# Kernel tuning notes

Measured on AMD Instinct MI355X. Metric: run time of the kernel, lower is better.

The kernel has to match this reference:

```python
import jax, jax.numpy as jnp
import numpy as np

EPS = 1e-5
GRID = (16, 16)
BLOCK = (16, 16)


def _ln(x):
    # LayerNorm over (C, H, W) per sample, affine = identity (fresh nn.LayerNorm each call)
    m = jnp.mean(x, axis=(1, 2, 3), keepdims=True)
    v = jnp.mean(jnp.square(x - m), axis=(1, 2, 3), keepdims=True)
    return (x - m) / jnp.sqrt(v + EPS)


def _gelu(x):
    return jax.nn.gelu(x, approximate=False)  # torch F.gelu default = exact erf


def _block(x, fh, fw):
    # NCHW -> [N, C, gh*gw, fh*fw]
    n, c, h, w = x.shape
    gh, gw = h // fh, w // fw
    return x.reshape(n, c, gh, fh, gw, fw).transpose(0, 1, 2, 4, 3, 5).reshape(n, c, gh * gw, fh * fw)


def _unblock(x, gh, gw, fh, fw):
    n, c, _, _ = x.shape
    return x.reshape(n, c, gh, gw, fh, fw).transpose(0, 1, 2, 4, 3, 5).reshape(n, c, gh * fh, gw * fw)


def _gating(x, w1, b1, w2, b2, w3, b3, w4, b4):
    # GetSpatialGatingWeights
    n, c, h, w = x.shape
    x = _ln(x)
    x = jnp.einsum('nchw,cd->ndhw', x, w1) + b1[None, :, None, None]  # C -> 2C
    x = _gelu(x)
    u, v = jnp.split(x, 2, axis=1)
    # grid MLP on u: mix across gh*gw grid positions
    gh, gw = GRID
    fh, fw = h // gh, w // gw
    u = _block(u, fh, fw)                                             # [n,c,G,P]
    u = jnp.einsum('ncgp,gd->ncdp', u, w2) + b2[None, None, :, None]
    u = _unblock(u, gh, gw, fh, fw)
    # block MLP on v: mix across fh*fw positions inside each block
    fh, fw = BLOCK
    gh, gw = h // fh, w // fw
    v = _block(v, fh, fw)
    v = jnp.einsum('ncgp,pd->ncgd', v, w3) + b3
    v = _unblock(v, gh, gw, fh, fw)
    x = jnp.concatenate([u, v], axis=1)
    return jnp.einsum('nchw,cd->ndhw', x, w4) + b4[None, :, None, None]  # 2C -> C


def _chan_lin(x, w, b):
    return jnp.einsum('nchw,cd->ndhw', x, w) + b[None, :, None, None]


def setup_inputs() -> dict:
    key = jax.random.key(0)
    ks = list(jax.random.split(key, 40))
    k = iter(ks)

    def rn(shape, s=0.02):
        return jax.random.normal(next(k), shape, dtype=jnp.float32) * s

    N, Cx, Cy, F, H, W = 8, 128, 256, 128, 128, 128
    G = GRID[0] * GRID[1]    # 256
    B = BLOCK[0] * BLOCK[1]  # 256
    inp = {
        'x': jax.random.normal(next(k), (N, Cx, H, W), dtype=jnp.float32),
        'y': jax.random.normal(next(k), (N, Cy, H // 2, W // 2), dtype=jnp.float32),
        'wt': rn((Cy, F, 2, 2)), 'bt': rn((F,)),
        'wc1': rn((Cx, F)), 'bc1': rn((F,)),
        'wc2': rn((F, F)), 'bc2': rn((F,)),
        'wl1': rn((F, F)), 'bl1': rn((F,)),
        'wl2': rn((F, F)), 'bl2': rn((F,)),
        'wl3': rn((F, F)), 'bl3': rn((F,)),
        'wl4': rn((F, F)), 'bl4': rn((F,)),
    }
    for p in ('g1', 'g2'):
        inp[p + '_w1'] = rn((F, 2 * F)); inp[p + '_b1'] = rn((2 * F,))
        inp[p + '_w2'] = rn((G, G));     inp[p + '_b2'] = rn((G,))
        inp[p + '_w3'] = rn((B, B));     inp[p + '_b3'] = rn((B,))
        inp[p + '_w4'] = rn((2 * F, F)); inp[p + '_b4'] = rn((F,))
    return inp


def reference(x, y, wt, bt, wc1, bc1, wc2, bc2, wl1, bl1, wl2, bl2, wl3, bl3, wl4, bl4,
              g1_w1, g1_b1, g1_w2, g1_b2, g1_w3, g1_b3, g1_w4, g1_b4,
              g2_w1, g2_b1, g2_w2, g2_b2, g2_w3, g2_b3, g2_w4, g2_b4):
    # ConvT_up: kernel=2, stride=2 (non-overlapping) + ReLU
    n, cy, hy, wy = y.shape
    fo = wt.shape[1]
    y = jnp.einsum('nchw,cokl->nohkwl', y, wt).reshape(n, fo, 2 * hy, 2 * wy) + bt[None, :, None, None]
    y = jax.nn.relu(y)
    # Conv1x1 (+ReLU) projections
    x = jax.nn.relu(_chan_lin(x, wc1, bc1))
    y = jax.nn.relu(_chan_lin(y, wc2, bc2))
    shortcut_x, shortcut_y = x, y
    # x branch
    x = _gelu(_chan_lin(_ln(x), wl1, bl1))
    gx = _gating(x, g1_w1, g1_b1, g1_w2, g1_b2, g1_w3, g1_b3, g1_w4, g1_b4)
    # y branch
    y = _gelu(_chan_lin(_ln(y), wl2, bl2))
    gy = _gating(y, g2_w1, g2_b1, g2_w2, g2_b2, g2_w3, g2_b3, g2_w4, g2_b4)
    # cross gating + residuals (dropout p=0.0 -> identity)
    y = _chan_lin(y * gx, wl3, bl3) + shortcut_y
    x = _chan_lin(x * gy, wl4, bl4) + y + shortcut_x
    return x, y
```

## Files before the change

### kernel.cpp

```cpp
#include <hip/hip_runtime.h>
#include <hip/hip_bf16.h>


typedef unsigned short u16;
typedef __bf16 bf16x8 __attribute__((ext_vector_type(8)));
typedef u16    u16x8  __attribute__((ext_vector_type(8)));
typedef u16    u16x4  __attribute__((ext_vector_type(4)));
typedef float  f32x4  __attribute__((ext_vector_type(4)));

__device__ __forceinline__ float bf2f(u16 u) {
  union { float f; unsigned int i; } v; v.i = ((unsigned int)u) << 16; return v.f;
}
__device__ __forceinline__ u16 f2bf(float f) {
  union { float f; unsigned int i; } v; v.f = f;
  unsigned int x = v.i;
  return (u16)((x + 0x7fffu + ((x >> 16) & 1u)) >> 16);
}
__device__ __forceinline__ f32x4 mfma16(u16x8 a, u16x8 b, f32x4 c) {
  return __builtin_amdgcn_mfma_f32_16x16x32_bf16(
      __builtin_bit_cast(bf16x8, a), __builtin_bit_cast(bf16x8, b), c, 0, 0, 0);
}
__device__ __forceinline__ float gelu_erf(float v) {
  return 0.5f * v * (1.0f + erff(v * 0.70710678118654752f));
}

__global__ __launch_bounds__(256) void prep_k(
    const float* __restrict__ wc1f, const float* __restrict__ wc2f,
    const float* __restrict__ wl1f, const float* __restrict__ wl2f,
    const float* __restrict__ wl3f, const float* __restrict__ wl4f,
    const float* __restrict__ g1w1, const float* __restrict__ g2w1,
    const float* __restrict__ g1w4, const float* __restrict__ g2w4,
    const float* __restrict__ g1w2, const float* __restrict__ g2w2,
    const float* __restrict__ g1w3, const float* __restrict__ g2w3,
    const float* __restrict__ wtf,
    u16* __restrict__ wb, float* __restrict__ cs, float* __restrict__ ps) {
  const int b = blockIdx.x, t = threadIdx.x;
  if (b < 384) {
    const float* src = b < 64 ? wc1f : b < 128 ? wc2f : b < 192 ? wl1f
                     : b < 256 ? wl2f : b < 320 ? wl3f : wl4f;
    const int w = b >> 6;
    const int i = ((b & 63) << 8) + t;
    const int d = i >> 7, c = i & 127;
    wb[w * 16384 + i] = f2bf(src[c * 128 + d]);
  } else if (b < 640) {
    const float* src = b < 512 ? g1w1 : g2w1;
    const int base = b < 512 ? 98304 : 131072;
    const int i = (((b - (b < 512 ? 384 : 512)) << 8) + t);
    const int d = i >> 7, c = i & 127;
    wb[base + i] = f2bf(src[c * 256 + d]);
  } else if (b < 896) {
    const float* src = b < 768 ? g1w4 : g2w4;
    const int base = b < 768 ? 163840 : 196608;
    const int i = (((b - (b < 768 ? 640 : 768)) << 8) + t);
    const int d = i >> 8, c = i & 255;
    wb[base + i] = f2bf(src[c * 128 + d]);
  } else if (b < 1920) {
    const int w = (b - 896) >> 8;
    const float* src = w == 0 ? g1w2 : w == 1 ? g2w2 : w == 2 ? g1w3 : g2w3;
    const int base = 229376 + w * 65536;
    const int i = (((b - 896) & 255) << 8) + t;
    const int d = i >> 8, g = i & 255;
    wb[base + i] = f2bf(src[g * 256 + d]);
  } else if (b < 2432) {
    const int i = ((b - 1920) << 8) + t;
    const int c = i & 255, r = i >> 8, o = r & 127, kl = r >> 7;
    wb[491520 + i] = f2bf(wtf[(c * 128 + o) * 4 + kl]);
  } else if (b < 2436) {
    const int w = b - 2432;
    const float* src = w == 0 ? wl1f : w == 1 ? wl2f : w == 2 ? g1w1 : g2w1;
    const int cout = w < 2 ? 128 : 256;
    if (t < cout) {
      float s = 0.f;
      for (int c = 0; c < 128; ++c) s += bf2f(f2bf(src[c * cout + t]));
      cs[w * 256 + t] = s;
    }
  } else {
    if (t < 64) ps[t] = 0.f;
  }
}

__global__ __launch_bounds__(256, 2) void gemmX_k(
    const float* __restrict__ X, const u16* __restrict__ Wt,
    const float* __restrict__ bias, u16* __restrict__ out,
    float* __restrict__ pso) {
  __shared__ u16 As[128 * 136];
  __shared__ float red[8];
  const int tid = threadIdx.x;
  const int m0 = blockIdx.x * 128;
  const int ns = m0 >> 14, pb = m0 & 16383;
  const int wid = tid >> 6, lane = tid & 63, fr = lane & 15, fg = lane >> 4;
  const int wmt = (wid & 1) * 64, wnc = (wid >> 1) * 64;

#pragma unroll
  for (int it = 0; it < 16; ++it) {
    const int idx = it * 256 + tid;
    const int c = idx & 127, t4 = idx >> 7;
    const f32x4 v = *(const f32x4*)(X + (((size_t)(ns * 128 + c)) << 14) + pb + t4 * 4);
#pragma unroll
    for (int r = 0; r < 4; ++r) As[(t4 * 4 + r) * 136 + c] = f2bf(v[r]);
  }
  __syncthreads();

  f32x4 acc[4][4] = {};
  const u16* Brow = Wt + (size_t)(wnc + fr) * 128;
  u16x8 a[4][4];
#pragma unroll
  for (int ks = 0; ks < 4; ++ks) {
    const int kb = ks * 32 + fg * 8;
#pragma unroll
    for (int i = 0; i < 4; ++i)
      a[ks][i] = *(const u16x8*)(As + (wmt + i * 16 + fr) * 136 + kb);
  }
#pragma unroll
  for (int ks = 0; ks < 4; ++ks) {
    const int kb = ks * 32 + fg * 8;
    u16x8 b_[4];
#pragma unroll
    for (int j = 0; j < 4; ++j)
      b_[j] = *(const u16x8*)(Brow + (size_t)j * 16 * 128 + kb);
#pragma unroll
    for (int i = 0; i < 4; ++i)
#pragma unroll
      for (int j = 0; j < 4; ++j) acc[i][j] = mfma16(b_[j], a[ks][i], acc[i][j]);
  }

  float s1 = 0.f, s2 = 0.f;
#pragma unroll
  for (int i = 0; i < 4; ++i) {
    const int token = m0 + wmt + i * 16 + fr;
#pragma unroll
    for (int j = 0; j < 4; ++j) {
      const int ch0 = wnc + j * 16 + fg * 4;
      const f32x4 bz = *(const f32x4*)(bias + ch0);
      f32x4 v = acc[i][j];
      u16x4 sv;
#pragma unroll
      for (int r = 0; r < 4; ++r) {
        v[r] = fmaxf(v[r] + bz[r], 0.f);
        s1 += v[r]; s2 += v[r] * v[r];
        sv[r] = f2bf(v[r]);
      }
      *(u16x4*)(out + (size_t)token * 128 + ch0) = sv;
    }
  }
#pragma unroll
  for (int off = 32; off > 0; off >>= 1) {
    s1 += __shfl_down(s1, off); s2 += __shfl_down(s2, off);
  }
  if (lane == 0) { red[wid] = s1; red[4 + wid] = s2; }
  __syncthreads();
  if (tid == 0)  atomicAdd(&pso[2 * ns],     red[0] + red[1] + red[2] + red[3]);
  if (tid == 64) atomicAdd(&pso[2 * ns + 1], red[4] + red[5] + red[6] + red[7]);
}

__global__ __launch_bounds__(256, 2) void gemmY2_k(
    const float* __restrict__ Y, const u16* __restrict__ Wtb,
    const float* __restrict__ bt, const u16* __restrict__ Wc2,
    const float* __restrict__ bc2, u16* __restrict__ out,
    float* __restrict__ pso) {
  __shared__ u16 As[64 * 256];
  __shared__ u16 Cs[64 * 136];
  __shared__ float red[8];
  const int tid = threadIdx.x;
  const int m0 = blockIdx.x * 64;
  const int ns = m0 >> 12, pb = m0 & 4095;
  const int wid = tid >> 6, lane = tid & 63, fr = lane & 15, fg = lane >> 4;
  const int tokg = (wid & 1) * 32;
  const int chg  = (wid >> 1) * 64;
  const int xorl = (fr & 7) << 4;

#pragma unroll
  for (int it = 0; it < 16; ++it) {
    const int idx = it * 256 + tid;
    const int c = idx & 255, t4 = idx >> 8;
    const f32x4 v = *(const f32x4*)(Y + (((size_t)(ns * 256 + c)) << 12) + pb + t4 * 4);
#pragma unroll
    for (int r = 0; r < 4; ++r) {
      const int tok = t4 * 4 + r;
      const int byte = (tok * 512 + c * 2) ^ ((tok & 7) << 4);
      *(u16*)((char*)As + byte) = f2bf(v[r]);
    }
  }
  __syncthreads();

  float s1 = 0.f, s2 = 0.f;
  for (int kl = 0; kl < 4; ++kl) {
    if (kl) __syncthreads();
    f32x4 acc1[2][4] = {};
    {
      const u16* Brow = Wtb + (size_t)(kl * 128 + chg + fr) * 256;
#pragma unroll
      for (int ks = 0; ks < 8; ++ks) {
        const int kb = ks * 32 + fg * 8;
        u16x8 a_[2], b_[4];
#pragma unroll
        for (int i = 0; i < 2; ++i) {
          const int tok = tokg + i * 16 + fr;
          const int byte = (tok * 512 + kb * 2) ^ xorl;
          a_[i] = *(const u16x8*)((const char*)As + byte);
        }
#pragma unroll
        for (int j = 0; j < 4; ++j)
          b_[j] = *(const u16x8*)(Brow + (size_t)j * 16 * 256 + kb);
#pragma unroll
        for (int i = 0; i < 2; ++i)
#pragma unroll
          for (int j = 0; j < 4; ++j) acc1[i][j] = mfma16(b_[j], a_[i], acc1[i][j]);
      }
    }
#pragma unroll
    for (int i = 0; i < 2; ++i) {
      const int tok = tokg + i * 16 + fr;
#pragma unroll
      for (int j = 0; j < 4; ++j) {
        const int o0 = chg + j * 16 + fg * 4;
        const f32x4 bz = *(const f32x4*)(bt + o0);
        u16x4 sv;
#pragma unroll
        for (int r = 0; r < 4; ++r) sv[r] = f2bf(fmaxf(acc1[i][j][r] + bz[r], 0.f));
        *(u16x4*)(Cs + tok * 136 + o0) = sv;
      }
    }
    __syncthreads();
    f32x4 acc2[2][4] = {};
    {
      const u16* Brow = Wc2 + (size_t)(chg + fr) * 128;
#pragma unroll
      for (int ks = 0; ks < 4; ++ks) {
        const int kb = ks * 32 + fg * 8;
        u16x8 a_[2], b_[4];
#pragma unroll
        for (int i = 0; i < 2; ++i)
          a_[i] = *(const u16x8*)(Cs + (tokg + i * 16 + fr) * 136 + kb);
#pragma unroll
        for (int j = 0; j < 4; ++j)
          b_[j] = *(const u16x8*)(Brow + (size_t)j * 16 * 128 + kb);
#pragma unroll
        for (int i = 0; i < 2; ++i)
#pragma unroll
          for (int j = 0; j < 4; ++j) acc2[i][j] = mfma16(b_[j], a_[i], acc2[i][j]);
      }
    }
#pragma unroll
    for (int i = 0; i < 2; ++i) {
      const int ytok = m0 + tokg + i * 16 + fr;
      const int hy = (ytok >> 6) & 63, wy = ytok & 63;
      const int opix = ((ns * 128 + 2 * hy + (kl >> 1)) << 7) + 2 * wy + (kl & 1);
#pragma unroll
      for (int j = 0; j < 4; ++j) {
        const int ch0 = chg + j * 16 + fg * 4;
        const f32x4 bz = *(const f32x4*)(bc2 + ch0);
        u16x4 sv;
#pragma unroll
        for (int r = 0; r < 4; ++r) {
          float v = fmaxf(acc2[i][j][r] + bz[r], 0.f);
          s1 += v; s2 += v * v;
          sv[r] = f2bf(v);
        }
        *(u16x4*)(out + (size_t)opix * 128 + ch0) = sv;
      }
    }
  }
#pragma unroll
  for (int off = 32; off > 0; off >>= 1) {
    s1 += __shfl_down(s1, off); s2 += __shfl_down(s2, off);
  }
  if (lane == 0) { red[wid] = s1; red[4 + wid] = s2; }
  __syncthreads();
  if (tid == 0)  atomicAdd(&pso[2 * ns],     red[0] + red[1] + red[2] + red[3]);
  if (tid == 64) atomicAdd(&pso[2 * ns + 1], red[4] + red[5] + red[6] + red[7]);
}

__global__ __launch_bounds__(256, 2) void gemm4d_k(
    const u16* __restrict__ Ay, const u16* __restrict__ Ax,
    const u16* __restrict__ Wty, const u16* __restrict__ Wtx,
    const float* __restrict__ by, const float* __restrict__ bx,
    float* __restrict__ ps,
    const float* __restrict__ csy, const float* __restrict__ csx,
    u16* __restrict__ oy, u16* __restrict__ ox) {
  __shared__ float red[8];
  const int br = blockIdx.y;
  const u16* A1 = br ? Ax : Ay;
  const u16* Wt = br ? Wtx : Wty;
  const float* bias = br ? bx : by;
  const float* pst = ps + (br ? 0 : 16);
  float* pso = ps + (br ? 32 : 48);
  const float* cs = br ? csx : csy;
  u16* out = br ? ox : oy;

  const int tid = threadIdx.x;
  const int m0 = blockIdx.x * 128;
  const int wid = tid >> 6, lane = tid & 63, fr = lane & 15, fg = lane >> 4;
  const int wmt = (wid & 1) * 64, wnc = (wid >> 1) * 64;

  f32x4 acc[4][4] = {};
  const u16* Arow = A1 + (size_t)(m0 + wmt + fr) * 128;
  const u16* Brow = Wt + (size_t)(wnc + fr) * 128;

  u16x8 a[4][4];
#pragma unroll
  for (int ks = 0; ks < 4; ++ks) {
    const int kb = ks * 32 + fg * 8;
#pragma unroll
    for (int i = 0; i < 4; ++i)
      a[ks][i] = *(const u16x8*)(Arow + (size_t)i * 16 * 128 + kb);
  }
#pragma unroll
  for (int ks = 0; ks < 4; ++ks) {
    const int kb = ks * 32 + fg * 8;
    u16x8 b_[4];
#pragma unroll
    for (int j = 0; j < 4; ++j)
      b_[j] = *(const u16x8*)(Brow + (size_t)j * 16 * 128 + kb);
#pragma unroll
    for (int i = 0; i < 4; ++i)
#pragma unroll
      for (int j = 0; j < 4; ++j) acc[i][j] = mfma16(b_[j], a[ks][i], acc[i][j]);
  }

  const int s = m0 >> 14;
  const float inv_n = 1.f / 2097152.f;
  const float mean = pst[2 * s] * inv_n;
  const float var = pst[2 * s + 1] * inv_n - mean * mean;
  const float alpha = rsqrtf(var + 1e-5f);
  const float beta = -mean * alpha;

  float s1 = 0.f, s2 = 0.f;
#pragma unroll
  for (int i = 0; i < 4; ++i) {
    const int token = m0 + wmt + i * 16 + fr;
#pragma unroll
    for (int j = 0; j < 4; ++j) {
      const int ch0 = wnc + j * 16 + fg * 4;
      const f32x4 bz = *(const f32x4*)(bias + ch0);
      const f32x4 csv = *(const f32x4*)(cs + ch0);
      f32x4 v = acc[i][j];
      u16x4 sv;
#pragma unroll
      for (int r = 0; r < 4; ++r) {
        v[r] = v[r] * alpha + beta * csv[r] + bz[r];
        v[r] = gelu_erf(v[r]);
        s1 += v[r]; s2 += v[r] * v[r];
        sv[r] = f2bf(v[r]);
      }
      *(u16x4*)(out + (size_t)token * 128 + ch0) = sv;
    }
  }
#pragma unroll
  for (int off = 32; off > 0; off >>= 1) {
    s1 += __shfl_down(s1, off); s2 += __shfl_down(s2, off);
  }
  if (lane == 0) { red[wid] = s1; red[4 + wid] = s2; }
  __syncthreads();
  if (tid == 0)  atomicAdd(&pso[2 * s],     red[0] + red[1] + red[2] + red[3]);
  if (tid == 64) atomicAdd(&pso[2 * s + 1], red[4] + red[5] + red[6] + red[7]);
}

template <int MODE>
__global__ __launch_bounds__(512, 2) void mlp3c_k(
    const u16* __restrict__ a1y, const u16* __restrict__ a1x,
    const u16* __restrict__ w1y, const u16* __restrict__ w1x,
    const float* __restrict__ b1y, const float* __restrict__ b1x,
    const float* __restrict__ ps,
    const float* __restrict__ csy, const float* __restrict__ csx,
    const u16* __restrict__ w2y, const u16* __restrict__ w2x,
    const float* __restrict__ b2y, const float* __restrict__ b2x,
    const u16* __restrict__ w4y, const u16* __restrict__ w4x,
    const float* __restrict__ b4y, const float* __restrict__ b4x,
    u16* __restrict__ goy, u16* __restrict__ gox) {
  __shared__ u16 Ts[34816];
  const int br = blockIdx.z;
  const u16* y1 = br ? a1x : a1y;
  const u16* w1b = br ? w1x : w1y;
  const float* b1 = br ? b1x : b1y;
  const float* pst = ps + (br ? 32 : 48);
  const float* csb = br ? csx : csy;
  const u16* w2b = br ? w2x : w2y;
  const float* b2 = br ? b2x : b2y;
  const u16* w4b = br ? w4x : w4y;
  const float* b4 = br ? b4x : b4y;
  u16* gout = br ? gox : goy;

  const int q2 = blockIdx.x, ns = blockIdx.y;
  const int tid = threadIdx.x;
  constexpr int coff = MODE ? 128 : 0;
  const int wid = tid >> 6, lane = tid & 63, fr = lane & 15, fg = lane >> 4;
  const int xorl = (fr & 7) << 4;

  int pbase, prow, pcol;
  if constexpr (MODE == 0) {
    pbase = ns * 16384 + (q2 >> 3) * 128 + (q2 & 7);
    prow = 1024; pcol = 8;
  } else {
    pbase = ns * 16384 + (q2 >> 3) * 2048 + (q2 & 7) * 16;
    prow = 128; pcol = 1;
  }
  auto pix = [&](int q) { return pbase + (q >> 4) * prow + (q & 15) * pcol; };

  {
    const int wgt = (wid >> 1) * 64;
    const int wc  = (wid & 1) * 64;
    const float inv_n = 1.f / 2097152.f;
    const float mean = pst[2 * ns] * inv_n;
    const float var = pst[2 * ns + 1] * inv_n - mean * mean;
    const float alpha = rsqrtf(var + 1e-5f);
    const float beta = -mean * alpha;

    f32x4 acc[4][4] = {};
    const u16* ar[4];
#pragma unroll
    for (int i = 0; i < 4; ++i)
      ar[i] = y1 + (size_t)pix(wgt + i * 16 + fr) * 128;
    const u16* br_ = w1b + (size_t)(coff + wc + fr) * 128;

    u16x8 a[4][4];
#pragma unroll
    for (int ks = 0; ks < 4; ++ks) {
      const int kb = ks * 32 + fg * 8;
#pragma unroll
      for (int i = 0; i < 4; ++i) a[ks][i] = *(const u16x8*)(ar[i] + kb);
    }
#pragma unroll
    for (int ks = 0; ks < 4; ++ks) {
      const int kb = ks * 32 + fg * 8;
      u16x8 b_[4];
#pragma unroll
      for (int j = 0; j < 4; ++j)
        b_[j] = *(const u16x8*)(br_ + (size_t)j * 16 * 128 + kb);
#pragma unroll
      for (int i = 0; i < 4; ++i)
#pragma unroll
        for (int j = 0; j < 4; ++j) acc[i][j] = mfma16(a[ks][i], b_[j], acc[i][j]);
    }
#pragma unroll
    for (int j = 0; j < 4; ++j) {
      const int c = wc + j * 16 + fr;
      const float cv = csb[coff + c];
      const float bz = b1[coff + c];
#pragma unroll
      for (int i = 0; i < 4; ++i) {
        const int g0 = wgt + i * 16 + fg * 4;
        u16x4 sv;
#pragma unroll
        for (int r = 0; r < 4; ++r)
          sv[r] = f2bf(gelu_erf(acc[i][j][r] * alpha + beta * cv + bz));
        const int byte = (c * 512 + g0 * 2) ^ xorl;
        *(u16x4*)((char*)Ts + byte) = sv;
      }
    }
  }
  __syncthreads();

  f32x4 accB[4][4];
  const int wcs = (wid >> 2) * 64;
  const int wds = (wid & 3) * 64;
  {
#pragma unroll
    for (int i = 0; i < 4; ++i)
#pragma unroll
      for (int j = 0; j < 4; ++j) accB[i][j] = f32x4{0.f, 0.f, 0.f, 0.f};
    const u16* br_ = w2b + (size_t)(wds + fr) * 256;
#pragma unroll
    for (int h = 0; h < 2; ++h) {
      u16x8 a[4][4];
#pragma unroll
      for (int ks = 0; ks < 4; ++ks) {
        const int kb = (h * 4 + ks) * 32 + fg * 8;
#pragma unroll
        for (int i = 0; i < 4; ++i) {
          const int c = wcs + i * 16 + fr;
          const int byte = (c * 512 + kb * 2) ^ xorl;
          a[ks][i] = *(const u16x8*)((const char*)Ts + byte);
        }
      }
#pragma unroll
      for (int ks = 0; ks < 4; ++ks) {
        const int kb = (h * 4 + ks) * 32 + fg * 8;
        u16x8 b_[4];
#pragma unroll
        for (int j = 0; j < 4; ++j)
          b_[j] = *(const u16x8*)(br_ + (size_t)j * 16 * 256 + kb);
#pragma unroll
        for (int i = 0; i < 4; ++i)
#pragma unroll
          for (int j = 0; j < 4; ++j) accB[i][j] = mfma16(a[ks][i], b_[j], accB[i][j]);
      }
    }
  }
  __syncthreads();

#pragma unroll
  for (int j = 0; j < 4; ++j) {
    const int d = wds + j * 16 + fr;
    const float bz = b2[d];
#pragma unroll
    for (int i = 0; i < 4; ++i) {
      const int c0 = wcs + i * 16 + fg * 4;
      u16x4 sv;
#pragma unroll
      for (int r = 0; r < 4; ++r) sv[r] = f2bf(accB[i][j][r] + bz);
      *(u16x4*)(Ts + d * 136 + c0) = sv;
    }
  }
  __syncthreads();

  {
    const int wp = (wid >> 1) * 64;
    const int wo = (wid & 1) * 64;
    f32x4 accC[4][4] = {};
    const u16* br_ = w4b + (size_t)(wo + fr) * 256 + coff;
#pragma unroll
    for (int ks = 0; ks < 4; ++ks) {
      const int kb = ks * 32 + fg * 8;
      u16x8 a_[4], b_[4];
#pragma unroll
      for (int i = 0; i < 4; ++i)
        a_[i] = *(const u16x8*)(Ts + (wp + i * 16 + fr) * 136 + kb);
#pragma unroll
      for (int j = 0; j < 4; ++j)
        b_[j] = *(const u16x8*)(br_ + (size_t)j * 16 * 256 + kb);
#pragma unroll
      for (int i = 0; i < 4; ++i)
#pragma unroll
        for (int j = 0; j < 4; ++j) accC[i][j] = mfma16(b_[j], a_[i], accC[i][j]);
    }
#pragma unroll
    for (int i = 0; i < 4; ++i) {
      const size_t pg = (size_t)pix(wp + i * 16 + fr) * 128;
#pragma unroll
      for (int j = 0; j < 4; ++j) {
        const int o0 = wo + j * 16 + fg * 4;
        f32x4 v = accC[i][j];
        u16x4 sv;
        if constexpr (MODE == 0) {
          const f32x4 bz = *(const f32x4*)(b4 + o0);
#pragma unroll
          for (int r = 0; r < 4; ++r) sv[r] = f2bf(v[r] + bz[r]);
        } else {
          const u16x4 pv = *(const u16x4*)(gout + pg + o0);
#pragma unroll
          for (int r = 0; r < 4; ++r) sv[r] = f2bf(v[r] + bf2f(pv[r]));
        }
        *(u16x4*)(gout + pg + o0) = sv;
      }
    }
  }
}

__global__ __launch_bounds__(256, 2) void dual5_k(
    const u16* __restrict__ y1, const u16* __restrict__ gx,
    const u16* __restrict__ x1, const u16* __restrict__ gy,
    const u16* __restrict__ w3b, const u16* __restrict__ w4b,
    const float* __restrict__ b3, const float* __restrict__ b4,
    const u16* __restrict__ y0, const u16* __restrict__ x0,
    float* __restrict__ outy, float* __restrict__ outx) {
  const int tid = threadIdx.x;
  const int m0 = blockIdx.x * 128;
  const int wid = tid >> 6, lane = tid & 63, fr = lane & 15, fg = lane >> 4;
  const int wmt = (wid & 1) * 64, wnc = (wid >> 1) * 64;

  f32x4 acc[4][4] = {};
  u16x4 y9[4][4];

  {
    const u16* Arow  = y1 + (size_t)(m0 + wmt + fr) * 128;
    const u16* Arow2 = gx + (size_t)(m0 + wmt + fr) * 128;
    const u16* Brow  = w3b + (size_t)(wnc + fr) * 128;
    u16x8 a[4][4], a2[4][4];
#pragma unroll
    for (int ks = 0; ks < 4; ++ks) {
      const int kb = ks * 32 + fg * 8;
#pragma unroll
      for (int i = 0; i < 4; ++i) {
        a[ks][i]  = *(const u16x8*)(Arow  + (size_t)i * 16 * 128 + kb);
        a2[ks][i] = *(const u16x8*)(Arow2 + (size_t)i * 16 * 128 + kb);
      }
    }
#pragma unroll
    for (int ks = 0; ks < 4; ++ks) {
      const int kb = ks * 32 + fg * 8;
      u16x8 b_[4];
#pragma unroll
      for (int j = 0; j < 4; ++j) b_[j] = *(const u16x8*)(Brow + (size_t)j * 16 * 128 + kb);
      u16x8 am[4];
#pragma unroll
      for (int i = 0; i < 4; ++i)
#pragma unroll
        for (int j = 0; j < 8; ++j) am[i][j] = f2bf(bf2f(a[ks][i][j]) * bf2f(a2[ks][i][j]));
#pragma unroll
      for (int i = 0; i < 4; ++i)
#pragma unroll
        for (int j = 0; j < 4; ++j) acc[i][j] = mfma16(b_[j], am[i], acc[i][j]);
    }
  }
  {
    u16x4 scv[4][4];
#pragma unroll
    for (int i = 0; i < 4; ++i) {
      const int token = m0 + wmt + i * 16 + fr;
#pragma unroll
      for (int j = 0; j < 4; ++j)
        scv[i][j] = *(const u16x4*)(y0 + (size_t)token * 128 + wnc + j * 16 + fg * 4);
    }
#pragma unroll
    for (int i = 0; i < 4; ++i) {
      const int token = m0 + wmt + i * 16 + fr;
      const int ns = token >> 14, p = token & 16383;
#pragma unroll
      for (int j = 0; j < 4; ++j) {
        const int ch0 = wnc + j * 16 + fg * 4;
        const f32x4 bz = *(const f32x4*)(b3 + ch0);
        f32x4 v = acc[i][j];
#pragma unroll
        for (int r = 0; r < 4; ++r) {
          v[r] += bz[r] + bf2f(scv[i][j][r]);
          outy[((size_t)(ns * 128 + ch0 + r) << 14) + p] = v[r];
          y9[i][j][r] = f2bf(v[r]);
        }
        acc[i][j] = f32x4{0.f, 0.f, 0.f, 0.f};
      }
    }
  }
  {
    const u16* Arow  = x1 + (size_t)(m0 + wmt + fr) * 128;
    const u16* Arow2 = gy + (size_t)(m0 + wmt + fr) * 128;
    const u16* Brow  = w4b + (size_t)(wnc + fr) * 128;
    u16x8 a[4][4], a2[4][4];
#pragma unroll
    for (int ks = 0; ks < 4; ++ks) {
      const int kb = ks * 32 + fg * 8;
#pragma unroll
      for (int i = 0; i < 4; ++i) {
        a[ks][i]  = *(const u16x8*)(Arow  + (size_t)i * 16 * 128 + kb);
        a2[ks][i] = *(const u16x8*)(Arow2 + (size_t)i * 16 * 128 + kb);
      }
    }
#pragma unroll
    for (int ks = 0; ks < 4; ++ks) {
      const int kb = ks * 32 + fg * 8;
      u16x8 b_[4];
#pragma unroll
      for (int j = 0; j < 4; ++j) b_[j] = *(const u16x8*)(Brow + (size_t)j * 16 * 128 + kb);
      u16x8 am[4];
#pragma unroll
      for (int i = 0; i < 4; ++i)
#pragma unroll
        for (int j = 0; j < 8; ++j) am[i][j] = f2bf(bf2f(a[ks][i][j]) * bf2f(a2[ks][i][j]));
#pragma unroll
      for (int i = 0; i < 4; ++i)
#pragma unroll
        for (int j = 0; j < 4; ++j) acc[i][j] = mfma16(b_[j], am[i], acc[i][j]);
    }
  }
  {
    u16x4 scv[4][4];
#pragma unroll
    for (int i = 0; i < 4; ++i) {
      const int token = m0 + wmt + i * 16 + fr;
#pragma unroll
      for (int j = 0; j < 4; ++j)
        scv[i][j] = *(const u16x4*)(x0 + (size_t)token * 128 + wnc + j * 16 + fg * 4);
    }
#pragma unroll
    for (int i = 0; i < 4; ++i) {
      const int token = m0 + wmt + i * 16 + fr;
      const int ns = token >> 14, p = token & 16383;
#pragma unroll
      for (int j = 0; j < 4; ++j) {
        const int ch0 = wnc + j * 16 + fg * 4;
        const f32x4 bz = *(const f32x4*)(b4 + ch0);
        f32x4 v = acc[i][j];
#pragma unroll
        for (int r = 0; r < 4; ++r) {
          v[r] += bz[r] + bf2f(y9[i][j][r]) + bf2f(scv[i][j][r]);
          outx[((size_t)(ns * 128 + ch0 + r) << 14) + p] = v[r];
        }
      }
    }
  }
}

extern "C" void kernel_launch(void* const* d_in, const int* in_sizes, int n_in,
                              void* d_out, int out_size, void* d_ws, size_t ws_size,
                              hipStream_t stream) {
  (void)in_sizes; (void)n_in; (void)out_size; (void)ws_size;
  const float* xf   = (const float*)d_in[0];
  const float* yf   = (const float*)d_in[1];
  const float* wtf  = (const float*)d_in[2];
  const float* btf  = (const float*)d_in[3];
  const float* wc1f = (const float*)d_in[4];
  const float* bc1f = (const float*)d_in[5];
  const float* wc2f = (const float*)d_in[6];
  const float* bc2f = (const float*)d_in[7];
  const float* wl1f = (const float*)d_in[8];
  const float* bl1f = (const float*)d_in[9];
  const float* wl2f = (const float*)d_in[10];
  const float* bl2f = (const float*)d_in[11];
  const float* wl3f = (const float*)d_in[12];
  const float* bl3f = (const float*)d_in[13];
  const float* wl4f = (const float*)d_in[14];
  const float* bl4f = (const float*)d_in[15];
  const float* g1w1 = (const float*)d_in[16];
  const float* g1b1 = (const float*)d_in[17];
  const float* g1w2 = (const float*)d_in[18];
  const float* g1b2 = (const float*)d_in[19];
  const float* g1w3 = (const float*)d_in[20];
  const float* g1b3 = (const float*)d_in[21];
  const float* g1w4 = (const float*)d_in[22];
  const float* g1b4 = (const float*)d_in[23];
  const float* g2w1 = (const float*)d_in[24];
  const float* g2b1 = (const float*)d_in[25];
  const float* g2w2 = (const float*)d_in[26];
  const float* g2b2 = (const float*)d_in[27];
  const float* g2w3 = (const float*)d_in[28];
  const float* g2b3 = (const float*)d_in[29];
  const float* g2w4 = (const float*)d_in[30];
  const float* g2b4 = (const float*)d_in[31];

  constexpr int T16 = 16777216;
  u16* WS  = (u16*)d_ws;
  u16* x0b = WS;
  u16* x1b = WS + (size_t)T16;
  u16* y0b = WS + (size_t)2 * T16;
  u16* y1b = WS + (size_t)3 * T16;
  u16* gyb = WS + (size_t)4 * T16;
  u16* gxb = WS + (size_t)5 * T16;
  float* fb = (float*)(WS + (size_t)6 * T16);
  float* cs = fb;
  float* ps = fb + 1024;
  u16* wb   = (u16*)(fb + 1024 + 64);
  float* ps0 = ps, *ps1 = ps + 16;

  const u16* wc1b = wb;
  const u16* wc2b = wb + 16384;
  const u16* wl1b = wb + 32768;
  const u16* wl2b = wb + 49152;
  const u16* wl3b = wb + 65536;
  const u16* wl4b = wb + 81920;
  const u16* g1w1b = wb + 98304;
  const u16* g2w1b = wb + 131072;
  const u16* g1w4b = wb + 163840;
  const u16* g2w4b = wb + 196608;
  const u16* g1w2b = wb + 229376;
  const u16* g2w2b = wb + 294912;
  const u16* g1w3b = wb + 360448;
  const u16* g2w3b = wb + 425984;
  const u16* wtb   = wb + 491520;

  float* outx = (float*)d_out;
  float* outy = (float*)d_out + (size_t)T16;

  const dim3 B256(256), B512(512);

  prep_k<<<dim3(2437), B256, 0, stream>>>(
      wc1f, wc2f, wl1f, wl2f, wl3f, wl4f, g1w1, g2w1, g1w4, g2w4,
      g1w2, g2w2, g1w3, g2w3, wtf, wb, cs, ps);

  gemmY2_k<<<dim3(512), B256, 0, stream>>>(yf, wtb, btf, wc2b, bc2f, y0b, ps1);
  gemmX_k<<<dim3(1024), B256, 0, stream>>>(xf, wc1b, bc1f, x0b, ps0);

  gemm4d_k<<<dim3(1024, 2), B256, 0, stream>>>(
      y0b, x0b, wl2b, wl1b, bl2f, bl1f, ps, cs + 256, cs, y1b, x1b);

  mlp3c_k<0><<<dim3(64, 8, 2), B512, 0, stream>>>(
      y1b, x1b, g2w1b, g1w1b, g2b1, g1b1, ps, cs + 768, cs + 512,
      g2w2b, g1w2b, g2b2, g1b2, g2w4b, g1w4b, g2b4, g1b4, gyb, gxb);
  mlp3c_k<1><<<dim3(64, 8, 2), B512, 0, stream>>>(
      y1b, x1b, g2w1b, g1w1b, g2b1, g1b1, ps, cs + 768, cs + 512,
      g2w3b, g1w3b, g2b3, g1b3, g2w4b, g1w4b, g2b4, g1b4, gyb, gxb);

  dual5_k<<<dim3(1024), B256, 0, stream>>>(
      y1b, gxb, x1b, gyb, wl3b, wl4b, bl3f, bl4f, y0b, x0b, outy, outx);
}
```

Before: 535.2 us.

## Merge input projection kernels and fold gating multiply into gating epilogue

The separate y (convT+conv1x1) and x (conv1x1) projection kernels become one launch with 1536 blocks, branching on block index, so the two independent workloads share the GPU. The cross-gating multiply (y1*gx, x1*gy) moves from the final dual GEMM's inner loop into the epilogue of the second gating-MLP pass, which writes the gated product directly. The final kernel then reads one activation tensor per branch instead of two and skips the per-element bf16 multiply. The cost is an extra read in the gating epilogue, plus one more bf16 rounding step before the multiply.

After: 517.5 us. 3.3% less time.

```diff
diff --git a/kernel.cpp b/kernel.cpp
--- a/kernel.cpp
+++ b/kernel.cpp
@@ -79,196 +79,195 @@
   }
 }
 
-__global__ __launch_bounds__(256, 2) void gemmX_k(
-    const float* __restrict__ X, const u16* __restrict__ Wt,
-    const float* __restrict__ bias, u16* __restrict__ out,
-    float* __restrict__ pso) {
-  __shared__ u16 As[128 * 136];
+__global__ __launch_bounds__(256, 2) void gemmYX_k(
+    const float* __restrict__ Y, const float* __restrict__ X,
+    const u16* __restrict__ Wtb, const float* __restrict__ bt,
+    const u16* __restrict__ Wc2, const float* __restrict__ bc2,
+    const u16* __restrict__ Wc1, const float* __restrict__ bc1,
+    u16* __restrict__ oy, u16* __restrict__ ox, float* __restrict__ ps) {
+  __shared__ u16 sm[25088];
   __shared__ float red[8];
   const int tid = threadIdx.x;
-  const int m0 = blockIdx.x * 128;
-  const int ns = m0 >> 14, pb = m0 & 16383;
   const int wid = tid >> 6, lane = tid & 63, fr = lane & 15, fg = lane >> 4;
-  const int wmt = (wid & 1) * 64, wnc = (wid >> 1) * 64;
-
-#pragma unroll
-  for (int it = 0; it < 16; ++it) {
-    const int idx = it * 256 + tid;
-    const int c = idx & 127, t4 = idx >> 7;
-    const f32x4 v = *(const f32x4*)(X + (((size_t)(ns * 128 + c)) << 14) + pb + t4 * 4);
-#pragma unroll
-    for (int r = 0; r < 4; ++r) As[(t4 * 4 + r) * 136 + c] = f2bf(v[r]);
-  }
-  __syncthreads();
-
-  f32x4 acc[4][4] = {};
-  const u16* Brow = Wt + (size_t)(wnc + fr) * 128;
-  u16x8 a[4][4];
-#pragma unroll
-  for (int ks = 0; ks < 4; ++ks) {
-    const int kb = ks * 32 + fg * 8;
-#pragma unroll
-    for (int i = 0; i < 4; ++i)
-      a[ks][i] = *(const u16x8*)(As + (wmt + i * 16 + fr) * 136 + kb);
-  }
-#pragma unroll
-  for (int ks = 0; ks < 4; ++ks) {
-    const int kb = ks * 32 + fg * 8;
-    u16x8 b_[4];
-#pragma unroll
-    for (int j = 0; j < 4; ++j)
-      b_[j] = *(const u16x8*)(Brow + (size_t)j * 16 * 128 + kb);
-#pragma unroll
-    for (int i = 0; i < 4; ++i)
-#pragma unroll
-      for (int j = 0; j < 4; ++j) acc[i][j] = mfma16(b_[j], a[ks][i], acc[i][j]);
-  }
-
-  float s1 = 0.f, s2 = 0.f;
-#pragma unroll
-  for (int i = 0; i < 4; ++i) {
-    const int token = m0 + wmt + i * 16 + fr;
-#pragma unroll
-    for (int j = 0; j < 4; ++j) {
-      const int ch0 = wnc + j * 16 + fg * 4;
-      const f32x4 bz = *(const f32x4*)(bias + ch0);
-      f32x4 v = acc[i][j];
-      u16x4 sv;
+
+  if (blockIdx.x < 512) {
+    u16* As = sm;
+    u16* Cs = sm + 16384;
+    float* pso = ps + 16;
+    const int m0 = blockIdx.x * 64;
+    const int ns = m0 >> 12, pb = m0 & 4095;
+    const int tokg = (wid & 1) * 32;
+    const int chg  = (wid >> 1) * 64;
+    const int xorl = (fr & 7) << 4;
+
+#pragma unroll
+    for (int it = 0; it < 16; ++it) {
+      const int idx = it * 256 + tid;
+      const int c = idx & 255, t4 = idx >> 8;
+      const f32x4 v = *(const f32x4*)(Y + (((size_t)(ns * 256 + c)) << 12) + pb + t4 * 4);
 #pragma unroll
       for (int r = 0; r < 4; ++r) {
-        v[r] = fmaxf(v[r] + bz[r], 0.f);
-        s1 += v[r]; s2 += v[r] * v[r];
-        sv[r] = f2bf(v[r]);
-      }
-      *(u16x4*)(out + (size_t)token * 128 + ch0) = sv;
-    }
-  }
-#pragma unroll
-  for (int off = 32; off > 0; off >>= 1) {
-    s1 += __shfl_down(s1, off); s2 += __shfl_down(s2, off);
-  }
-  if (lane == 0) { red[wid] = s1; red[4 + wid] = s2; }
-  __syncthreads();
-  if (tid == 0)  atomicAdd(&pso[2 * ns],     red[0] + red[1] + red[2] + red[3]);
-  if (tid == 64) atomicAdd(&pso[2 * ns + 1], red[4] + red[5] + red[6] + red[7]);
-}
-
-__global__ __launch_bounds__(256, 2) void gemmY2_k(
-    const float* __restrict__ Y, const u16* __restrict__ Wtb,
-    const float* __restrict__ bt, const u16* __restrict__ Wc2,
-    const float* __restrict__ bc2, u16* __restrict__ out,
-    float* __restrict__ pso) {
-  __shared__ u16 As[64 * 256];
-  __shared__ u16 Cs[64 * 136];
-  __shared__ float red[8];
-  const int tid = threadIdx.x;
-  const int m0 = blockIdx.x * 64;
-  const int ns = m0 >> 12, pb = m0 & 4095;
-  const int wid = tid >> 6, lane = tid & 63, fr = lane & 15, fg = lane >> 4;
-  const int tokg = (wid & 1) * 32;
-  const int chg  = (wid >> 1) * 64;
-  const int xorl = (fr & 7) << 4;
-
-#pragma unroll
-  for (int it = 0; it < 16; ++it) {
-    const int idx = it * 256 + tid;
-    const int c = idx & 255, t4 = idx >> 8;
-    const f32x4 v = *(const f32x4*)(Y + (((size_t)(ns * 256 + c)) << 12) + pb + t4 * 4);
-#pragma unroll
-    for (int r = 0; r < 4; ++r) {
-      const int tok = t4 * 4 + r;
-      const int byte = (tok * 512 + c * 2) ^ ((tok & 7) << 4);
-      *(u16*)((char*)As + byte) = f2bf(v[r]);
-    }
-  }
-  __syncthreads();
-
-  float s1 = 0.f, s2 = 0.f;
-  for (int kl = 0; kl < 4; ++kl) {
-    if (kl) __syncthreads();
-    f32x4 acc1[2][4] = {};
-    {
-      const u16* Brow = Wtb + (size_t)(kl * 128 + chg + fr) * 256;
-#pragma unroll
-      for (int ks = 0; ks < 8; ++ks) {
-        const int kb = ks * 32 + fg * 8;
-        u16x8 a_[2], b_[4];
-#pragma unroll
-        for (int i = 0; i < 2; ++i) {
-          const int tok = tokg + i * 16 + fr;
-          const int byte = (tok * 512 + kb * 2) ^ xorl;
-          a_[i] = *(const u16x8*)((const char*)As + byte);
-        }
-#pragma unroll
-        for (int j = 0; j < 4; ++j)
-          b_[j] = *(const u16x8*)(Brow + (size_t)j * 16 * 256 + kb);
-#pragma unroll
-        for (int i = 0; i < 2; ++i)
-#pragma unroll
-          for (int j = 0; j < 4; ++j) acc1[i][j] = mfma16(b_[j], a_[i], acc1[i][j]);
-      }
-    }
-#pragma unroll
-    for (int i = 0; i < 2; ++i) {
-      const int tok = tokg + i * 16 + fr;
+        const int tok = t4 * 4 + r;
+        const int byte = (tok * 512 + c * 2) ^ ((tok & 7) << 4);
+        *(u16*)((char*)As + byte) = f2bf(v[r]);
+      }
+    }
+    __syncthreads();
+
+    float s1 = 0.f, s2 = 0.f;
+    for (int kl = 0; kl < 4; ++kl) {
+      if (kl) __syncthreads();
+      f32x4 acc1[2][4] = {};
+      {
+        const u16* Brow = Wtb + (size_t)(kl * 128 + chg + fr) * 256;
+#pragma unroll
+        for (int ks = 0; ks < 8; ++ks) {
+          const int kb = ks * 32 + fg * 8;
+          u16x8 a_[2], b_[4];
+#pragma unroll
+          for (int i = 0; i < 2; ++i) {
+            const int tok = tokg + i * 16 + fr;
+            const int byte = (tok * 512 + kb * 2) ^ xorl;
+            a_[i] = *(const u16x8*)((const char*)As + byte);
+          }
+#pragma unroll
+          for (int j = 0; j < 4; ++j)
+            b_[j] = *(const u16x8*)(Brow + (size_t)j * 16 * 256 + kb);
+#pragma unroll
+          for (int i = 0; i < 2; ++i)
+#pragma unroll
+            for (int j = 0; j < 4; ++j) acc1[i][j] = mfma16(b_[j], a_[i], acc1[i][j]);
+        }
+      }
+#pragma unroll
+      for (int i = 0; i < 2; ++i) {
+        const int tok = tokg + i * 16 + fr;
+#pragma unroll
+        for (int j = 0; j < 4; ++j) {
+          const int o0 = chg + j * 16 + fg * 4;
+          const f32x4 bz = *(const f32x4*)(bt + o0);
+          u16x4 sv;
+#pragma unroll
+          for (int r = 0; r < 4; ++r) sv[r] = f2bf(fmaxf(acc1[i][j][r] + bz[r], 0.f));
+          *(u16x4*)(Cs + tok * 136 + o0) = sv;
+        }
+      }
+      __syncthreads();
+      f32x4 acc2[2][4] = {};
+      {
+        const u16* Brow = Wc2 + (size_t)(chg + fr) * 128;
+#pragma unroll
+        for (int ks = 0; ks < 4; ++ks) {
+          const int kb = ks * 32 + fg * 8;
+          u16x8 a_[2], b_[4];
+#pragma unroll
+          for (int i = 0; i < 2; ++i)
+            a_[i] = *(const u16x8*)(Cs + (tokg + i * 16 + fr) * 136 + kb);
+#pragma unroll
+          for (int j = 0; j < 4; ++j)
+            b_[j] = *(const u16x8*)(Brow + (size_t)j * 16 * 128 + kb);
+#pragma unroll
+          for (int i = 0; i < 2; ++i)
+#pragma unroll
+            for (int j = 0; j < 4; ++j) acc2[i][j] = mfma16(b_[j], a_[i], acc2[i][j]);
+        }
+      }
+#pragma unroll
+      for (int i = 0; i < 2; ++i) {
+        const int ytok = m0 + tokg + i * 16 + fr;
+        const int hy = (ytok >> 6) & 63, wy = ytok & 63;
+        const int opix = ((ns * 128 + 2 * hy + (kl >> 1)) << 7) + 2 * wy + (kl & 1);
+#pragma unroll
+        for (int j = 0; j < 4; ++j) {
+          const int ch0 = chg + j * 16 + fg * 4;
+          const f32x4 bz = *(const f32x4*)(bc2 + ch0);
+          u16x4 sv;
+#pragma unroll
+          for (int r = 0; r < 4; ++r) {
+            float v = fmaxf(acc2[i][j][r] + bz[r], 0.f);
+            s1 += v; s2 += v * v;
+            sv[r] = f2bf(v);
+          }
+          *(u16x4*)(oy + (size_t)opix * 128 + ch0) = sv;
+        }
+      }
+    }
+#pragma unroll
+    for (int off = 32; off > 0; off >>= 1) {
+      s1 += __shfl_down(s1, off); s2 += __shfl_down(s2, off);
+    }
+    if (lane == 0) { red[wid] = s1; red[4 + wid] = s2; }
+    __syncthreads();
+    if (tid == 0)  atomicAdd(&pso[2 * ns],     red[0] + red[1] + red[2] + red[3]);
+    if (tid == 64) atomicAdd(&pso[2 * ns + 1], red[4] + red[5] + red[6] + red[7]);
+  } else {
+    u16* As = sm;
+    float* pso = ps;
+    const int m0 = (blockIdx.x - 512) * 128;
+    const int ns = m0 >> 14, pb = m0 & 16383;
+    const int wmt = (wid & 1) * 64, wnc = (wid >> 1) * 64;
+
+#pragma unroll
+    for (int it = 0; it < 16; ++it) {
+      const int idx = it * 256 + tid;
+      const int c = idx & 127, t4 = idx >> 7;
+      const f32x4 v = *(const f32x4*)(X + (((size_t)(ns * 128 + c)) << 14) + pb + t4 * 4);
+#pragma unroll
+      for (int r = 0; r < 4; ++r) As[(t4 * 4 + r) * 136 + c] = f2bf(v[r]);
+    }
+    __syncthreads();
+
+    f32x4 acc[4][4] = {};
+    const u16* Brow = Wc1 + (size_t)(wnc + fr) * 128;
+    u16x8 a[4][4];
+#pragma unroll
+    for (int ks = 0; ks < 4; ++ks) {
+      const int kb = ks * 32 + fg * 8;
+#pragma unroll
+      for (int i = 0; i < 4; ++i)
+        a[ks][i] = *(const u16x8*)(As + (wmt + i * 16 + fr) * 136 + kb);
+    }
+#pragma unroll
+    for (int ks = 0; ks < 4; ++ks) {
+      const int kb = ks * 32 + fg * 8;
+      u16x8 b_[4];
+#pragma unroll
+      for (int j = 0; j < 4; ++j)
+        b_[j] = *(const u16x8*)(Brow + (size_t)j * 16 * 128 + kb);
+#pragma unroll
+      for (int i = 0; i < 4; ++i)
+#pragma unroll
+        for (int j = 0; j < 4; ++j) acc[i][j] = mfma16(b_[j], a[ks][i], acc[i][j]);
+    }
+
+    float s1 = 0.f, s2 = 0.f;
+#pragma unroll
+    for (int i = 0; i < 4; ++i) {
+      const int token = m0 + wmt + i * 16 + fr;
 #pragma unroll
       for (int j = 0; j < 4; ++j) {
-        const int o0 = chg + j * 16 + fg * 4;
-        const f32x4 bz = *(const f32x4*)(bt + o0);
+        const int ch0 = wnc + j * 16 + fg * 4;
+        const f32x4 bz = *(const f32x4*)(bc1 + ch0);
+        f32x4 v = acc[i][j];
         u16x4 sv;
 #pragma unroll
-        for (int r = 0; r < 4; ++r) sv[r] = f2bf(fmaxf(acc1[i][j][r] + bz[r], 0.f));
-        *(u16x4*)(Cs + tok * 136 + o0) = sv;
-      }
-    }
+        for (int r = 0; r < 4; ++r) {
+          v[r] = fmaxf(v[r] + bz[r], 0.f);
+          s1 += v[r]; s2 += v[r] * v[r];
+          sv[r] = f2bf(v[r]);
+        }
+        *(u16x4*)(ox + (size_t)token * 128 + ch0) = sv;
+      }
+    }
+#pragma unroll
+    for (int off = 32; off > 0; off >>= 1) {
+      s1 += __shfl_down(s1, off); s2 += __shfl_down(s2, off);
+    }
+    if (lane == 0) { red[wid] = s1; red[4 + wid] = s2; }
     __syncthreads();
-    f32x4 acc2[2][4] = {};
-    {
-      const u16* Brow = Wc2 + (size_t)(chg + fr) * 128;
-#pragma unroll
-      for (int ks = 0; ks < 4; ++ks) {
-        const int kb = ks * 32 + fg * 8;
-        u16x8 a_[2], b_[4];
-#pragma unroll
-        for (int i = 0; i < 2; ++i)
-          a_[i] = *(const u16x8*)(Cs + (tokg + i * 16 + fr) * 136 + kb);
-#pragma unroll
-        for (int j = 0; j < 4; ++j)
-          b_[j] = *(const u16x8*)(Brow + (size_t)j * 16 * 128 + kb);
-#pragma unroll
-        for (int i = 0; i < 2; ++i)
-#pragma unroll
-          for (int j = 0; j < 4; ++j) acc2[i][j] = mfma16(b_[j], a_[i], acc2[i][j]);
-      }
-    }
-#pragma unroll
-    for (int i = 0; i < 2; ++i) {
-      const int ytok = m0 + tokg + i * 16 + fr;
-      const int hy = (ytok >> 6) & 63, wy = ytok & 63;
-      const int opix = ((ns * 128 + 2 * hy + (kl >> 1)) << 7) + 2 * wy + (kl & 1);
-#pragma unroll
-      for (int j = 0; j < 4; ++j) {
-        const int ch0 = chg + j * 16 + fg * 4;
-        const f32x4 bz = *(const f32x4*)(bc2 + ch0);
-        u16x4 sv;
-#pragma unroll
-        for (int r = 0; r < 4; ++r) {
-          float v = fmaxf(acc2[i][j][r] + bz[r], 0.f);
-          s1 += v; s2 += v * v;
-          sv[r] = f2bf(v);
-        }
-        *(u16x4*)(out + (size_t)opix * 128 + ch0) = sv;
-      }
-    }
-  }
-#pragma unroll
-  for (int off = 32; off > 0; off >>= 1) {
-    s1 += __shfl_down(s1, off); s2 += __shfl_down(s2, off);
-  }
-  if (lane == 0) { red[wid] = s1; red[4 + wid] = s2; }
-  __syncthreads();
-  if (tid == 0)  atomicAdd(&pso[2 * ns],     red[0] + red[1] + red[2] + red[3]);
-  if (tid == 64) atomicAdd(&pso[2 * ns + 1], red[4] + red[5] + red[6] + red[7]);
+    if (tid == 0)  atomicAdd(&pso[2 * ns],     red[0] + red[1] + red[2] + red[3]);
+    if (tid == 64) atomicAdd(&pso[2 * ns + 1], red[4] + red[5] + red[6] + red[7]);
+  }
 }
 
 __global__ __launch_bounds__(256, 2) void gemm4d_k(
@@ -371,6 +370,7 @@
   __shared__ u16 Ts[34816];
   const int br = blockIdx.z;
   const u16* y1 = br ? a1x : a1y;
+  const u16* mulp = br ? a1y : a1x;
   const u16* w1b = br ? w1x : w1y;
   const float* b1 = br ? b1x : b1y;
   const float* pst = ps + (br ? 32 : 48);
@@ -538,8 +538,10 @@
           for (int r = 0; r < 4; ++r) sv[r] = f2bf(v[r] + bz[r]);
         } else {
           const u16x4 pv = *(const u16x4*)(gout + pg + o0);
-#pragma unroll
-          for (int r = 0; r < 4; ++r) sv[r] = f2bf(v[r] + bf2f(pv[r]));
+          const u16x4 mv = *(const u16x4*)(mulp + pg + o0);
+#pragma unroll
+          for (int r = 0; r < 4; ++r)
+            sv[r] = f2bf((v[r] + bf2f(pv[r])) * bf2f(mv[r]));
         }
         *(u16x4*)(gout + pg + o0) = sv;
       }
@@ -548,8 +550,7 @@
 }
 
 __global__ __launch_bounds__(256, 2) void dual5_k(
-    const u16* __restrict__ y1, const u16* __restrict__ gx,
-    const u16* __restrict__ x1, const u16* __restrict__ gy,
+    const u16* __restrict__ y1g, const u16* __restrict__ x1g,
     const u16* __restrict__ w3b, const u16* __restrict__ w4b,
     const float* __restrict__ b3, const float* __restrict__ b4,
     const u16* __restrict__ y0, const u16* __restrict__ x0,
@@ -563,18 +564,15 @@
   u16x4 y9[4][4];
 
   {
-    const u16* Arow  = y1 + (size_t)(m0 + wmt + fr) * 128;
-    const u16* Arow2 = gx + (size_t)(m0 + wmt + fr) * 128;
-    const u16* Brow  = w3b + (size_t)(wnc + fr) * 128;
-    u16x8 a[4][4], a2[4][4];
-#pragma unroll
-    for (int ks = 0; ks < 4; ++ks) {
-      const int kb = ks * 32 + fg * 8;
-#pragma unroll
-      for (int i = 0; i < 4; ++i) {
-        a[ks][i]  = *(const u16x8*)(Arow  + (size_t)i * 16 * 128 + kb);
-        a2[ks][i] = *(const u16x8*)(Arow2 + (size_t)i * 16 * 128 + kb);
-      }
+    const u16* Arow = y1g + (size_t)(m0 + wmt + fr) * 128;
+    const u16* Brow = w3b + (size_t)(wnc + fr) * 128;
+    u16x8 a[4][4];
+#pragma unroll
+    for (int ks = 0; ks < 4; ++ks) {
+      const int kb = ks * 32 + fg * 8;
+#pragma unroll
+      for (int i = 0; i < 4; ++i)
+        a[ks][i] = *(const u16x8*)(Arow + (size_t)i * 16 * 128 + kb);
     }
 #pragma unroll
     for (int ks = 0; ks < 4; ++ks) {
@@ -582,15 +580,10 @@
       u16x8 b_[4];
 #pragma unroll
       for (int j = 0; j < 4; ++j) b_[j] = *(const u16x8*)(Brow + (size_t)j * 16 * 128 + kb);
-      u16x8 am[4];
-#pragma unroll
-      for (int i = 0; i < 4; ++i)
-#pragma unroll
-        for (int j = 0; j < 8; ++j) am[i][j] = f2bf(bf2f(a[ks][i][j]) * bf2f(a2[ks][i][j]));
-#pragma unroll
-      for (int i = 0; i < 4; ++i)
-#pragma unroll
-        for (int j = 0; j < 4; ++j) acc[i][j] = mfma16(b_[j], am[i], acc[i][j]);
+#pragma unroll
+      for (int i = 0; i < 4; ++i)
+#pragma unroll
+        for (int j = 0; j < 4; ++j) acc[i][j] = mfma16(b_[j], a[ks][i], acc[i][j]);
     }
   }
   {
@@ -622,18 +615,15 @@
     }
   }
   {
-    const u16* Arow  = x1 + (size_t)(m0 + wmt + fr) * 128;
-    const u16* Arow2 = gy + (size_t)(m0 + wmt + fr) * 128;
-    const u16* Brow  = w4b + (size_t)(wnc + fr) * 128;
-    u16x8 a[4][4], a2[4][4];
-#pragma unroll
-    for (int ks = 0; ks < 4; ++ks) {
-      const int kb = ks * 32 + fg * 8;
-#pragma unroll
-      for (int i = 0; i < 4; ++i) {
-        a[ks][i]  = *(const u16x8*)(Arow  + (size_t)i * 16 * 128 + kb);
-        a2[ks][i] = *(const u16x8*)(Arow2 + (size_t)i * 16 * 128 + kb);
-      }
+    const u16* Arow = x1g + (size_t)(m0 + wmt + fr) * 128;
+    const u16* Brow = w4b + (size_t)(wnc + fr) * 128;
+    u16x8 a[4][4];
+#pragma unroll
+    for (int ks = 0; ks < 4; ++ks) {
+      const int kb = ks * 32 + fg * 8;
+#pragma unroll
+      for (int i = 0; i < 4; ++i)
+        a[ks][i] = *(const u16x8*)(Arow + (size_t)i * 16 * 128 + kb);
     }
 #pragma unroll
     for (int ks = 0; ks < 4; ++ks) {
@@ -641,15 +631,10 @@
       u16x8 b_[4];
 #pragma unroll
       for (int j = 0; j < 4; ++j) b_[j] = *(const u16x8*)(Brow + (size_t)j * 16 * 128 + kb);
-      u16x8 am[4];
-#pragma unroll
-      for (int i = 0; i < 4; ++i)
-#pragma unroll
-        for (int j = 0; j < 8; ++j) am[i][j] = f2bf(bf2f(a[ks][i][j]) * bf2f(a2[ks][i][j]));
-#pragma unroll
-      for (int i = 0; i < 4; ++i)
-#pragma unroll
-        for (int j = 0; j < 4; ++j) acc[i][j] = mfma16(b_[j], am[i], acc[i][j]);
+#pragma unroll
+      for (int i = 0; i < 4; ++i)
+#pragma unroll
+        for (int j = 0; j < 4; ++j) acc[i][j] = mfma16(b_[j], a[ks][i], acc[i][j]);
     }
   }
   {
@@ -729,7 +714,6 @@
   float* cs = fb;
   float* ps = fb + 1024;
   u16* wb   = (u16*)(fb + 1024 + 64);
-  float* ps0 = ps, *ps1 = ps + 16;
 
   const u16* wc1b = wb;
   const u16* wc2b = wb + 16384;
@@ -756,8 +740,8 @@
       wc1f, wc2f, wl1f, wl2f, wl3f, wl4f, g1w1, g2w1, g1w4, g2w4,
       g1w2, g2w2, g1w3, g2w3, wtf, wb, cs, ps);
 
-  gemmY2_k<<<dim3(512), B256, 0, stream>>>(yf, wtb, btf, wc2b, bc2f, y0b, ps1);
-  gemmX_k<<<dim3(1024), B256, 0, stream>>>(xf, wc1b, bc1f, x0b, ps0);
+  gemmYX_k<<<dim3(1536), B256, 0, stream>>>(
+      yf, xf, wtb, btf, wc2b, bc2f, wc1b, bc1f, y0b, x0b, ps);
 
   gemm4d_k<<<dim3(1024, 2), B256, 0, stream>>>(
       y0b, x0b, wl2b, wl1b, bl2f, bl1f, ps, cs + 256, cs, y1b, x1b);
@@ -770,5 +754,5 @@
       g2w3b, g1w3b, g2b3, g1b3, g2w4b, g1w4b, g2b4, g1b4, gyb, gxb);
 
   dual5_k<<<dim3(1024), B256, 0, stream>>>(
-      y1b, gxb, x1b, gyb, wl3b, wl4b, bl3f, bl4f, y0b, x0b, outy, outx);
-}
+      gxb, gyb, wl3b, wl4b, bl3f, bl4f, y0b, x0b, outy, outx);
+}
```
